# Performance work log

Hardware: AMD Instinct MI355X
Metric: run time of the kernel (lower is better)

The kernel has to match this reference:

```python
import jax, jax.numpy as jnp
import numpy as np

SCORE_THRESH = 0.05
NMS_THRESH = 0.5
MAX_DET = 100
BBOX_XFORM_CLIP = float(np.log(1000.0 / 16.0))


def decode_boxes(proposals, deltas):
    # proposals, deltas: [..., 4] in (x1, y1, x2, y2) / (dx, dy, dw, dh)
    w = proposals[..., 2] - proposals[..., 0]
    h = proposals[..., 3] - proposals[..., 1]
    cx = proposals[..., 0] + 0.5 * w
    cy = proposals[..., 1] + 0.5 * h
    dx, dy = deltas[..., 0], deltas[..., 1]
    dw = jnp.minimum(deltas[..., 2], BBOX_XFORM_CLIP)
    dh = jnp.minimum(deltas[..., 3], BBOX_XFORM_CLIP)
    pcx = dx * w + cx
    pcy = dy * h + cy
    pw = jnp.exp(dw) * w
    ph = jnp.exp(dh) * h
    return jnp.stack([pcx - 0.5 * pw, pcy - 0.5 * ph,
                      pcx + 0.5 * pw, pcy + 0.5 * ph], axis=-1)


def iou_matrix(boxes):
    # boxes: [N, 4] -> [N, N] pairwise IoU
    area = (boxes[:, 2] - boxes[:, 0]) * (boxes[:, 3] - boxes[:, 1])
    lt = jnp.maximum(boxes[:, None, :2], boxes[None, :, :2])
    rb = jnp.minimum(boxes[:, None, 2:], boxes[None, :, 2:])
    wh = jnp.clip(rb - lt, 0.0)
    inter = wh[..., 0] * wh[..., 1]
    union = area[:, None] + area[None, :] - inter
    return inter / (union + 1e-9)


def nms_single(boxes, scores, labels, valid):
    # Greedy batched NMS for one image with fixed shapes.
    N = boxes.shape[0]
    neg = jnp.finfo(scores.dtype).min
    s = jnp.where(valid, scores, neg)
    # class-offset trick (torchvision batched_nms)
    max_coord = jnp.max(jnp.where(valid[:, None], boxes, 0.0))
    obox = boxes + labels.astype(boxes.dtype)[:, None] * (max_coord + 1.0)
    order = jnp.argsort(-s)
    obox_s = obox[order]
    s_s = s[order]
    valid_s = valid[order]
    iou = iou_matrix(obox_s)  # [N, N]
    idxs = jnp.arange(N)

    def body(i, suppressed):
        keep_i = jnp.logical_and(~suppressed[i], valid_s[i])
        return suppressed | (keep_i & (iou[i] > NMS_THRESH) & (idxs > i))

    suppressed = jax.lax.fori_loop(0, N, body, jnp.zeros((N,), bool))
    keep = (~suppressed) & valid_s
    final_s = jnp.where(keep, s_s, neg)
    top_s, top_i = jax.lax.top_k(final_s, MAX_DET)
    sel = order[top_i]
    valid_out = keep[top_i]
    out_boxes = jnp.where(valid_out[:, None], boxes[sel], 0.0)
    out_scores = jnp.where(valid_out, top_s, 0.0)
    out_labels = jnp.where(valid_out, labels[sel], -1)
    return out_boxes, out_scores, out_labels


def setup_inputs() -> dict:
    key = jax.random.key(0)
    k1, k2, k3, k4, k5 = jax.random.split(key, 5)
    B, N, C = 16, 1024, 91
    class_logits = jax.random.normal(k1, (B, N, C), dtype=jnp.float32)
    bbox_deltas = 0.1 * jax.random.normal(k2, (B, N, C * 4), dtype=jnp.float32)
    xy = jax.random.uniform(k3, (B, N, 2), dtype=jnp.float32) * 800.0
    wh = jax.random.uniform(k4, (B, N, 2), dtype=jnp.float32) * 200.0 + 1.0
    roi_proposals = jnp.concatenate([xy, xy + wh], axis=-1)
    image_sizes = jax.random.randint(k5, (B, 2), 512, 1333).astype(jnp.int32)  # (h, w)
    return {"class_logits": class_logits, "bbox_deltas": bbox_deltas,
            "roi_proposals": roi_proposals, "image_sizes": image_sizes}


def reference(class_logits, bbox_deltas, roi_proposals, image_sizes):
    B, N, C = class_logits.shape
    probs_all = jax.nn.softmax(class_logits, axis=-1)
    scores = jnp.max(probs_all, axis=-1)          # [B, N]
    labels = jnp.argmax(probs_all, axis=-1)       # [B, N]
    valid = (labels > 0) & (scores > SCORE_THRESH)
    # gather per-class deltas (same as the 4*idx .. 4*idx+3 gather)
    deltas = bbox_deltas.reshape(B, N, C, 4)
    matched = jnp.take_along_axis(deltas, labels[:, :, None, None], axis=2)[:, :, 0, :]
    boxes = decode_boxes(roi_proposals, matched)
    hw = image_sizes.astype(boxes.dtype)          # (h, w)
    bound = jnp.stack([hw[:, 1], hw[:, 0], hw[:, 1], hw[:, 0]], axis=-1)[:, None, :]
    boxes = jnp.clip(boxes, 0.0, bound)
    out_boxes, out_scores, out_labels = jax.vmap(nms_single)(boxes, scores, labels, valid)
    return out_boxes, out_scores, out_labels
```

## Files before the change

### kernel.cpp

```cpp
#include <hip/hip_runtime.h>
#include <math.h>

#define NN 1024
#define CC 91
#define MAXDET 100
typedef unsigned long long ull;
#define SENT 0xFFFFFFFFFFFFFFFFULL

struct alignas(16) D4 { double x, y, z, w; };

__global__ __launch_bounds__(256) void k1_decode(
    const float* __restrict__ logits, const float* __restrict__ deltas,
    const float* __restrict__ props,  const int* __restrict__ imsz,
    D4* __restrict__ dbox, double* __restrict__ score64,
    int* __restrict__ label, ull* __restrict__ skeyG, ull* __restrict__ keptKey)
{
    int lane = threadIdx.x & 63;
    int wv   = threadIdx.x >> 6;
    int pid  = blockIdx.x * 4 + wv;
    const float* lg = logits + (size_t)pid * CC;

    float v0 = lg[lane];
    float v1 = (lane < CC - 64) ? lg[64 + lane] : -INFINITY;
    float m; int idx;
    if (v0 >= v1) { m = v0; idx = lane; } else { m = v1; idx = 64 + lane; }
    #pragma unroll
    for (int off = 32; off > 0; off >>= 1) {
        float om = __shfl_xor(m, off);
        int   oi = __shfl_xor(idx, off);
        if (om > m || (om == m && oi < idx)) { m = om; idx = oi; }
    }
    double e = exp((double)v0 - (double)m);
    if (lane < CC - 64) e += exp((double)v1 - (double)m);
    #pragma unroll
    for (int off = 32; off > 0; off >>= 1) e += __shfl_xor(e, off);

    if (lane == 0) {
        double score = 1.0 / e;
        int lbl = idx;
        int vld = (lbl > 0 && score > 0.05) ? 1 : 0;
        float4 d = ((const float4*)deltas)[(size_t)pid * CC + lbl];
        float4 p = ((const float4*)props)[pid];
        double w  = (double)p.z - (double)p.x;
        double h  = (double)p.w - (double)p.y;
        double cx = (double)p.x + 0.5 * w;
        double cy = (double)p.y + 0.5 * h;
        const double CLIPV = 4.135166556742356;
        double dw = fmin((double)d.z, CLIPV), dh = fmin((double)d.w, CLIPV);
        double pcx = (double)d.x * w + cx, pcy = (double)d.y * h + cy;
        double pw = exp(dw) * w, ph = exp(dh) * h;
        double x1 = pcx - 0.5 * pw, y1 = pcy - 0.5 * ph;
        double x2 = pcx + 0.5 * pw, y2 = pcy + 0.5 * ph;
        int b = pid >> 10;
        double bw = (double)imsz[b * 2 + 1], bh = (double)imsz[b * 2 + 0];
        x1 = fmin(fmax(x1, 0.0), bw); y1 = fmin(fmax(y1, 0.0), bh);
        x2 = fmin(fmax(x2, 0.0), bw); y2 = fmin(fmax(y2, 0.0), bh);
        dbox[pid]    = D4{x1, y1, x2, y2};
        score64[pid] = score;
        label[pid]   = vld ? lbl : 0;
        double seff = vld ? score : -1e300;
        ull u   = (ull)__double_as_longlong(seff);
        ull asc = (u >> 63) ? ~u : (u | 0x8000000000000000ULL);
        skeyG[pid]   = (~asc & ~1023ULL) | (ull)(pid & 1023);
        keptKey[pid] = SENT;
    }
}

__global__ __launch_bounds__(256) void k2_nms(
    const D4* __restrict__ dbox, const int* __restrict__ label,
    const ull* __restrict__ skeyG, ull* __restrict__ keptKey)
{
    __shared__ int sMemb[4 * 64];
    __shared__ int sPosR[4 * 64];
    __shared__ ull sKeyR[4 * 64];
    int lane = threadIdx.x & 63, wv = threadIdx.x >> 6;
    int gw = blockIdx.x * 4 + wv;
    int b  = gw / 90;
    int c  = 1 + gw % 90;
    int base = b * NN;
    ull lmlt = (lane == 0) ? 0ULL : ((1ULL << lane) - 1ULL);

    int nmem = 0;
    for (int w = 0; w < 16; ++w) {
        int p = w * 64 + lane;
        bool match = (label[base + p] == c);
        ull mb = __ballot(match);
        if (match) {
            int slot = nmem + (int)__popcll(mb & lmlt);
            if (slot < 64) sMemb[wv * 64 + slot] = p;
        }
        nmem += (int)__popcll(mb);
        if (nmem >= 64) break;
    }
    int n = nmem < 64 ? nmem : 64;
    if (n == 0) return;

    int p = sMemb[wv * 64 + (lane < n ? lane : 0)];
    ull key = skeyG[base + p];
    int rank = 0;
    for (int j = 0; j < n; ++j) {
        ull kj = __shfl(key, j);
        rank += (int)(kj < key);
    }
    if (lane < n) { sPosR[wv * 64 + rank] = p; sKeyR[wv * 64 + rank] = key; }
    int rl  = wv * 64 + (lane < n ? lane : 0);
    int p2  = sPosR[rl];
    ull k2v = sKeyR[rl];

    D4 bx = dbox[base + p2];
    double ma = (bx.z - bx.x) * (bx.w - bx.y);
    ull pm = 0;
    for (int j = 0; j < n; ++j) {
        double jx = __shfl(bx.x, j), jy = __shfl(bx.y, j);
        double jz = __shfl(bx.z, j), jw = __shfl(bx.w, j);
        double ja = __shfl(ma, j);
        double xx1 = fmax(bx.x, jx), yy1 = fmax(bx.y, jy);
        double xx2 = fmin(bx.z, jz), yy2 = fmin(bx.w, jw);
        double iw = fmax(xx2 - xx1, 0.0), ih = fmax(yy2 - yy1, 0.0);
        double inter = iw * ih;
        bool hit = (inter > 0.5 * (ma + ja - inter + 1e-9)) && (j < lane);
        pm |= ((ull)hit) << j;
    }
    bool act = lane < n;
    ull avail = __ballot(act);
    ull keptw = 0; bool supp = false;
    while (avail) {
        int k0 = __builtin_ctzll(avail);
        keptw |= 1ULL << k0;
        supp = supp || ((pm >> k0) & 1ULL);
        avail &= ~__ballot(supp);
        avail &= ~((2ULL << k0) - 1ULL);
    }
    if (act && ((keptw >> lane) & 1ULL)) keptKey[base + p2] = k2v;
}

__global__ __launch_bounds__(1024) void k3_top(
    const D4* __restrict__ dbox, const double* __restrict__ score64,
    const int* __restrict__ label, const ull* __restrict__ keptKey,
    float* __restrict__ out)
{
    __shared__ ull sRun[NN];
    int b = blockIdx.x, t = threadIdx.x;
    int lane = t & 63, wv = t >> 6;
    int base = b * NN;

    ull key = keptKey[base + t];
    for (int k = 2; k <= 64; k <<= 1)
        for (int j = k >> 1; j > 0; j >>= 1) {
            ull part = __shfl_xor(key, j);
            bool keepMin = ((lane & j) == 0) == ((lane & k) == 0);
            ull mn = key < part ? key : part;
            ull mx = key < part ? part : key;
            key = keepMin ? mn : mx;
        }
    sRun[wv * 64 + lane] = key;
    __syncthreads();

    if (wv < 8) {
        ull a  = sRun[wv * 128 + lane];
        ull bb = sRun[wv * 128 + 64 + lane];
        ull br = __shfl(bb, 63 - lane);
        ull lo = a < br ? a : br;
        ull hi = a < br ? br : a;
        #pragma unroll
        for (int j = 32; j > 0; j >>= 1) {
            bool km = ((lane & j) == 0);
            ull pl = __shfl_xor(lo, j);
            lo = km ? (lo < pl ? lo : pl) : (lo < pl ? pl : lo);
            ull ph = __shfl_xor(hi, j);
            hi = km ? (hi < ph ? hi : ph) : (hi < ph ? ph : hi);
        }
        sRun[wv * 128 + lane] = lo;
        sRun[wv * 128 + 64 + lane] = hi;
    }
    for (int nm = 4; nm >= 1; nm >>= 1) {
        __syncthreads();
        ull Alo = 0, Ahi = 0, Blo = 0, Bhi = 0;
        if (wv < nm) {
            Alo = sRun[wv * 256 + lane];
            Ahi = sRun[wv * 256 + 64 + lane];
            Blo = sRun[wv * 256 + 128 + lane];
            Bhi = sRun[wv * 256 + 192 + lane];
        }
        __syncthreads();
        if (wv < nm) {
            ull rBhi = __shfl(Bhi, 63 - lane);
            ull rBlo = __shfl(Blo, 63 - lane);
            ull Mlo = Alo < rBhi ? Alo : rBhi;
            ull Mhi = Ahi < rBlo ? Ahi : rBlo;
            ull l2 = Mlo < Mhi ? Mlo : Mhi;
            ull h2 = Mlo < Mhi ? Mhi : Mlo;
            #pragma unroll
            for (int j = 32; j > 0; j >>= 1) {
                bool km = ((lane & j) == 0);
                ull pl = __shfl_xor(l2, j);
                l2 = km ? (l2 < pl ? l2 : pl) : (l2 < pl ? pl : l2);
                ull ph = __shfl_xor(h2, j);
                h2 = km ? (h2 < ph ? h2 : ph) : (h2 < ph ? ph : h2);
            }
            sRun[wv * 128 + lane] = l2;
            sRun[wv * 128 + 64 + lane] = h2;
        }
    }
    if (wv == 0) {
        float* oBox   = out;
        float* oScore = out + 6400;
        float* oLabel = out + 8000;
        #pragma unroll
        for (int rsel = 0; rsel < 2; ++rsel) {
            int rank = rsel * 64 + lane;
            if (rank < MAXDET) {
                ull kf = sRun[rsel * 64 + lane];
                int q = b * MAXDET + rank;
                if (kf == SENT) {
                    oBox[q * 4 + 0] = 0.f; oBox[q * 4 + 1] = 0.f;
                    oBox[q * 4 + 2] = 0.f; oBox[q * 4 + 3] = 0.f;
                    oScore[q] = 0.f;
                    oLabel[q] = -1.f;
                } else {
                    int p = (int)(kf & 1023ULL);
                    D4 bx = dbox[base + p];
                    oBox[q * 4 + 0] = (float)bx.x; oBox[q * 4 + 1] = (float)bx.y;
                    oBox[q * 4 + 2] = (float)bx.z; oBox[q * 4 + 3] = (float)bx.w;
                    oScore[q] = (float)score64[base + p];
                    oLabel[q] = (float)label[base + p];
                }
            }
        }
    }
}

extern "C" void kernel_launch(void* const* d_in, const int* in_sizes, int n_in,
                              void* d_out, int out_size, void* d_ws, size_t ws_size,
                              hipStream_t stream) {
    const float* logits = (const float*)d_in[0];
    const float* deltas = (const float*)d_in[1];
    const float* props  = (const float*)d_in[2];
    const int*   imsz   = (const int*)d_in[3];
    char* ws = (char*)d_ws;
    D4*     dbox    = (D4*)(ws + 0);
    double* score64 = (double*)(ws + 524288);
    int*    label   = (int*)(ws + 655360);
    ull*    skeyG   = (ull*)(ws + 720896);
    ull*    keptKey = (ull*)(ws + 851968);
    float* out = (float*)d_out;

    k1_decode<<<dim3(4096), dim3(256), 0, stream>>>(logits, deltas, props, imsz,
                                                    dbox, score64, label, skeyG, keptKey);
    k2_nms<<<dim3(360), dim3(256), 0, stream>>>(dbox, label, skeyG, keptKey);
    k3_top<<<dim3(16), dim3(1024), 0, stream>>>(dbox, score64, label, keptKey, out);
}
```

Before: 102.5 us.

## Fuse per-class NMS into the per-image top-k kernel using shared memory

Merges the per-class NMS kernel into the per-image top-k kernel. Labels and keys are staged in LDS, and kept keys are written to shared memory instead of a global buffer. This removes one launch and the global keptKey init, write and read. In exchange, NMS work now runs on 16 blocks, with each wave looping over several classes serially, which reduces parallelism.

```diff
diff --git a/kernel.cpp b/kernel.cpp
--- a/kernel.cpp
+++ b/kernel.cpp
@@ -13,7 +13,7 @@
     const float* __restrict__ logits, const float* __restrict__ deltas,
     const float* __restrict__ props,  const int* __restrict__ imsz,
     D4* __restrict__ dbox, double* __restrict__ score64,
-    int* __restrict__ label, ull* __restrict__ skeyG, ull* __restrict__ keptKey)
+    int* __restrict__ label, ull* __restrict__ skeyG)
 {
     int lane = threadIdx.x & 63;
     int wv   = threadIdx.x >> 6;
@@ -61,90 +61,88 @@
         double seff = vld ? score : -1e300;
         ull u   = (ull)__double_as_longlong(seff);
         ull asc = (u >> 63) ? ~u : (u | 0x8000000000000000ULL);
-        skeyG[pid]   = (~asc & ~1023ULL) | (ull)(pid & 1023);
-        keptKey[pid] = SENT;
+        skeyG[pid] = (~asc & ~1023ULL) | (ull)(pid & 1023);
     }
 }
 
-__global__ __launch_bounds__(256) void k2_nms(
-    const D4* __restrict__ dbox, const int* __restrict__ label,
-    const ull* __restrict__ skeyG, ull* __restrict__ keptKey)
-{
-    __shared__ int sMemb[4 * 64];
-    __shared__ int sPosR[4 * 64];
-    __shared__ ull sKeyR[4 * 64];
-    int lane = threadIdx.x & 63, wv = threadIdx.x >> 6;
-    int gw = blockIdx.x * 4 + wv;
-    int b  = gw / 90;
-    int c  = 1 + gw % 90;
-    int base = b * NN;
-    ull lmlt = (lane == 0) ? 0ULL : ((1ULL << lane) - 1ULL);
-
-    int nmem = 0;
-    for (int w = 0; w < 16; ++w) {
-        int p = w * 64 + lane;
-        bool match = (label[base + p] == c);
-        ull mb = __ballot(match);
-        if (match) {
-            int slot = nmem + (int)__popcll(mb & lmlt);
-            if (slot < 64) sMemb[wv * 64 + slot] = p;
-        }
-        nmem += (int)__popcll(mb);
-        if (nmem >= 64) break;
-    }
-    int n = nmem < 64 ? nmem : 64;
-    if (n == 0) return;
-
-    int p = sMemb[wv * 64 + (lane < n ? lane : 0)];
-    ull key = skeyG[base + p];
-    int rank = 0;
-    for (int j = 0; j < n; ++j) {
-        ull kj = __shfl(key, j);
-        rank += (int)(kj < key);
-    }
-    if (lane < n) { sPosR[wv * 64 + rank] = p; sKeyR[wv * 64 + rank] = key; }
-    int rl  = wv * 64 + (lane < n ? lane : 0);
-    int p2  = sPosR[rl];
-    ull k2v = sKeyR[rl];
-
-    D4 bx = dbox[base + p2];
-    double ma = (bx.z - bx.x) * (bx.w - bx.y);
-    ull pm = 0;
-    for (int j = 0; j < n; ++j) {
-        double jx = __shfl(bx.x, j), jy = __shfl(bx.y, j);
-        double jz = __shfl(bx.z, j), jw = __shfl(bx.w, j);
-        double ja = __shfl(ma, j);
-        double xx1 = fmax(bx.x, jx), yy1 = fmax(bx.y, jy);
-        double xx2 = fmin(bx.z, jz), yy2 = fmin(bx.w, jw);
-        double iw = fmax(xx2 - xx1, 0.0), ih = fmax(yy2 - yy1, 0.0);
-        double inter = iw * ih;
-        bool hit = (inter > 0.5 * (ma + ja - inter + 1e-9)) && (j < lane);
-        pm |= ((ull)hit) << j;
-    }
-    bool act = lane < n;
-    ull avail = __ballot(act);
-    ull keptw = 0; bool supp = false;
-    while (avail) {
-        int k0 = __builtin_ctzll(avail);
-        keptw |= 1ULL << k0;
-        supp = supp || ((pm >> k0) & 1ULL);
-        avail &= ~__ballot(supp);
-        avail &= ~((2ULL << k0) - 1ULL);
-    }
-    if (act && ((keptw >> lane) & 1ULL)) keptKey[base + p2] = k2v;
-}
-
-__global__ __launch_bounds__(1024) void k3_top(
+__global__ __launch_bounds__(1024) void k23_nms_top(
     const D4* __restrict__ dbox, const double* __restrict__ score64,
-    const int* __restrict__ label, const ull* __restrict__ keptKey,
+    const int* __restrict__ label, const ull* __restrict__ skeyG,
     float* __restrict__ out)
 {
-    __shared__ ull sRun[NN];
+    __shared__ int sLbl[NN];
+    __shared__ ull sKey[NN];
+    __shared__ ull sKept[NN];
+    __shared__ int sMemb[16 * 64];
+    __shared__ int sPosR[16 * 64];
+    __shared__ ull sKeyR[16 * 64];
     int b = blockIdx.x, t = threadIdx.x;
     int lane = t & 63, wv = t >> 6;
     int base = b * NN;
 
-    ull key = keptKey[base + t];
+    sLbl[t]  = label[base + t];
+    sKey[t]  = skeyG[base + t];
+    sKept[t] = SENT;
+    __syncthreads();
+
+    ull lmlt = (lane == 0) ? 0ULL : ((1ULL << lane) - 1ULL);
+    for (int c = 1 + wv; c <= 90; c += 16) {
+        int nmem = 0;
+        for (int w = 0; w < 16; ++w) {
+            int p = w * 64 + lane;
+            bool match = (sLbl[p] == c);
+            ull mb = __ballot(match);
+            if (match) {
+                int slot = nmem + (int)__popcll(mb & lmlt);
+                if (slot < 64) sMemb[wv * 64 + slot] = p;
+            }
+            nmem += (int)__popcll(mb);
+            if (nmem >= 64) break;
+        }
+        int n = nmem < 64 ? nmem : 64;
+        if (n == 0) continue;
+
+        int p = sMemb[wv * 64 + (lane < n ? lane : 0)];
+        ull key = sKey[p];
+        int rank = 0;
+        for (int j = 0; j < n; ++j) {
+            ull kj = __shfl(key, j);
+            rank += (int)(kj < key);
+        }
+        if (lane < n) { sPosR[wv * 64 + rank] = p; sKeyR[wv * 64 + rank] = key; }
+        int rl  = wv * 64 + (lane < n ? lane : 0);
+        int p2  = sPosR[rl];
+        ull k2v = sKeyR[rl];
+
+        D4 bx = dbox[base + p2];
+        double ma = (bx.z - bx.x) * (bx.w - bx.y);
+        ull pm = 0;
+        for (int j = 0; j < n; ++j) {
+            double jx = __shfl(bx.x, j), jy = __shfl(bx.y, j);
+            double jz = __shfl(bx.z, j), jw = __shfl(bx.w, j);
+            double ja = __shfl(ma, j);
+            double xx1 = fmax(bx.x, jx), yy1 = fmax(bx.y, jy);
+            double xx2 = fmin(bx.z, jz), yy2 = fmin(bx.w, jw);
+            double iw = fmax(xx2 - xx1, 0.0), ih = fmax(yy2 - yy1, 0.0);
+            double inter = iw * ih;
+            bool hit = (inter > 0.5 * (ma + ja - inter + 1e-9)) && (j < lane);
+            pm |= ((ull)hit) << j;
+        }
+        bool act = lane < n;
+        ull avail = __ballot(act);
+        ull keptw = 0; bool supp = false;
+        while (avail) {
+            int k0 = __builtin_ctzll(avail);
+            keptw |= 1ULL << k0;
+            supp = supp || ((pm >> k0) & 1ULL);
+            avail &= ~__ballot(supp);
+            avail &= ~((2ULL << k0) - 1ULL);
+        }
+        if (act && ((keptw >> lane) & 1ULL)) sKept[p2] = k2v;
+    }
+    __syncthreads();
+
+    ull key = sKept[t];
     for (int k = 2; k <= 64; k <<= 1)
         for (int j = k >> 1; j > 0; j >>= 1) {
             ull part = __shfl_xor(key, j);
@@ -153,12 +151,13 @@
             ull mx = key < part ? part : key;
             key = keepMin ? mn : mx;
         }
-    sRun[wv * 64 + lane] = key;
+    __syncthreads();
+    sKept[wv * 64 + lane] = key;
     __syncthreads();
 
     if (wv < 8) {
-        ull a  = sRun[wv * 128 + lane];
-        ull bb = sRun[wv * 128 + 64 + lane];
+        ull a  = sKept[wv * 128 + lane];
+        ull bb = sKept[wv * 128 + 64 + lane];
         ull br = __shfl(bb, 63 - lane);
         ull lo = a < br ? a : br;
         ull hi = a < br ? br : a;
@@ -170,17 +169,17 @@
             ull ph = __shfl_xor(hi, j);
             hi = km ? (hi < ph ? hi : ph) : (hi < ph ? ph : hi);
         }
-        sRun[wv * 128 + lane] = lo;
-        sRun[wv * 128 + 64 + lane] = hi;
+        sKept[wv * 128 + lane] = lo;
+        sKept[wv * 128 + 64 + lane] = hi;
     }
     for (int nm = 4; nm >= 1; nm >>= 1) {
         __syncthreads();
         ull Alo = 0, Ahi = 0, Blo = 0, Bhi = 0;
         if (wv < nm) {
-            Alo = sRun[wv * 256 + lane];
-            Ahi = sRun[wv * 256 + 64 + lane];
-            Blo = sRun[wv * 256 + 128 + lane];
-            Bhi = sRun[wv * 256 + 192 + lane];
+            Alo = sKept[wv * 256 + lane];
+            Ahi = sKept[wv * 256 + 64 + lane];
+            Blo = sKept[wv * 256 + 128 + lane];
+            Bhi = sKept[wv * 256 + 192 + lane];
         }
         __syncthreads();
         if (wv < nm) {
@@ -198,8 +197,8 @@
                 ull ph = __shfl_xor(h2, j);
                 h2 = km ? (h2 < ph ? h2 : ph) : (h2 < ph ? ph : h2);
             }
-            sRun[wv * 128 + lane] = l2;
-            sRun[wv * 128 + 64 + lane] = h2;
+            sKept[wv * 128 + lane] = l2;
+            sKept[wv * 128 + 64 + lane] = h2;
         }
     }
     if (wv == 0) {
@@ -210,7 +209,7 @@
         for (int rsel = 0; rsel < 2; ++rsel) {
             int rank = rsel * 64 + lane;
             if (rank < MAXDET) {
-                ull kf = sRun[rsel * 64 + lane];
+                ull kf = sKept[rsel * 64 + lane];
                 int q = b * MAXDET + rank;
                 if (kf == SENT) {
                     oBox[q * 4 + 0] = 0.f; oBox[q * 4 + 1] = 0.f;
@@ -223,7 +222,7 @@
                     oBox[q * 4 + 0] = (float)bx.x; oBox[q * 4 + 1] = (float)bx.y;
                     oBox[q * 4 + 2] = (float)bx.z; oBox[q * 4 + 3] = (float)bx.w;
                     oScore[q] = (float)score64[base + p];
-                    oLabel[q] = (float)label[base + p];
+                    oLabel[q] = (float)sLbl[p];
                 }
             }
         }
@@ -242,11 +241,9 @@
     double* score64 = (double*)(ws + 524288);
     int*    label   = (int*)(ws + 655360);
     ull*    skeyG   = (ull*)(ws + 720896);
-    ull*    keptKey = (ull*)(ws + 851968);
     float* out = (float*)d_out;
 
     k1_decode<<<dim3(4096), dim3(256), 0, stream>>>(logits, deltas, props, imsz,
-                                                    dbox, score64, label, skeyG, keptKey);
-    k2_nms<<<dim3(360), dim3(256), 0, stream>>>(dbox, label, skeyG, keptKey);
-    k3_top<<<dim3(16), dim3(1024), 0, stream>>>(dbox, score64, label, keptKey, out);
+                                                    dbox, score64, label, skeyG);
+    k23_nms_top<<<dim3(16), dim3(1024), 0, stream>>>(dbox, score64, label, skeyG, out);
 }
```

Result: slower. 129.9 us (+26.7%).
